# Optimization experiments

Measured on AMD Instinct MI355X. Metric: run time of the kernel, lower is better.

Reference implementation:

```python
import jax, jax.numpy as jnp
import numpy as np

B, C, H, W = 1, 320, 64, 64
HEADS, DH = 8, 40            # inner_dim = 320
CTX_LEN, CTX_DIM = 77, 768
FF_MULT = 4
GN_GROUPS, GN_EPS = 32, 1e-6
LN_EPS = 1e-5
SCALE = DH ** -0.5
WSTD = 0.02


def setup_inputs() -> dict:
    key = jax.random.key(0)
    ks = iter(jax.random.split(key, 32))
    rn = lambda *s: jax.random.normal(next(ks), s, dtype=jnp.float32)
    D = HEADS * DH  # 320
    inp = {
        'hidden_states': rn(B, C, H, W),
        'encoder_hidden_states': rn(B, CTX_LEN, CTX_DIM),
        'gn_g': jnp.ones((C,), jnp.float32), 'gn_b': jnp.zeros((C,), jnp.float32),
        'pi_w': rn(C, D) * WSTD, 'pi_b': jnp.zeros((D,), jnp.float32),
        'n1_g': jnp.ones((D,), jnp.float32), 'n1_b': jnp.zeros((D,), jnp.float32),
        'a1_q': rn(D, D) * WSTD, 'a1_k': rn(D, D) * WSTD, 'a1_v': rn(D, D) * WSTD,
        'a1_o': rn(D, D) * WSTD, 'a1_ob': jnp.zeros((D,), jnp.float32),
        'n2_g': jnp.ones((D,), jnp.float32), 'n2_b': jnp.zeros((D,), jnp.float32),
        'a2_q': rn(D, D) * WSTD, 'a2_k': rn(CTX_DIM, D) * WSTD, 'a2_v': rn(CTX_DIM, D) * WSTD,
        'a2_o': rn(D, D) * WSTD, 'a2_ob': jnp.zeros((D,), jnp.float32),
        'n3_g': jnp.ones((D,), jnp.float32), 'n3_b': jnp.zeros((D,), jnp.float32),
        'ff_w1': rn(D, 2 * FF_MULT * D) * WSTD, 'ff_b1': jnp.zeros((2 * FF_MULT * D,), jnp.float32),
        'ff_w2': rn(FF_MULT * D, D) * WSTD, 'ff_b2': jnp.zeros((D,), jnp.float32),
        'po_w': rn(D, C) * WSTD, 'po_b': jnp.zeros((C,), jnp.float32),
    }
    return inp


def _group_norm(x, g, b):
    # x: [B,C,H,W]
    Bx, Cx, Hx, Wx = x.shape
    xr = x.reshape(Bx, GN_GROUPS, Cx // GN_GROUPS, Hx, Wx)
    mu = xr.mean(axis=(2, 3, 4), keepdims=True)
    var = xr.var(axis=(2, 3, 4), keepdims=True)
    xr = (xr - mu) * jax.lax.rsqrt(var + GN_EPS)
    x = xr.reshape(Bx, Cx, Hx, Wx)
    return x * g[None, :, None, None] + b[None, :, None, None]


def _layer_norm(x, g, b):
    mu = x.mean(-1, keepdims=True)
    var = x.var(-1, keepdims=True)
    return (x - mu) * jax.lax.rsqrt(var + LN_EPS) * g + b


def _attention(x, ctx, wq, wk, wv, wo, bo):
    # x: [B,S,D]; ctx: [B,T,Dc]. Same math as the torch sliced loop
    # (the 2-row slicing changes only execution order, not values).
    Bx, S, D = x.shape
    q = (x @ wq).reshape(Bx, S, HEADS, DH)
    k = (ctx @ wk).reshape(Bx, -1, HEADS, DH)
    v = (ctx @ wv).reshape(Bx, -1, HEADS, DH)
    s = jnp.einsum('bihd,bjhd->bhij', q, k) * SCALE
    p = jax.nn.softmax(s, axis=-1)
    o = jnp.einsum('bhij,bjhd->bihd', p, v).reshape(Bx, S, D)
    return o @ wo + bo


def reference(hidden_states, encoder_hidden_states, gn_g, gn_b, pi_w, pi_b,
              n1_g, n1_b, a1_q, a1_k, a1_v, a1_o, a1_ob,
              n2_g, n2_b, a2_q, a2_k, a2_v, a2_o, a2_ob,
              n3_g, n3_b, ff_w1, ff_b1, ff_w2, ff_b2, po_w, po_b):
    residual = hidden_states
    h = _group_norm(hidden_states, gn_g, gn_b)
    # proj_in: 1x1 conv == per-pixel linear; to [B, HW, D]
    h = jnp.einsum('bchw,cd->bhwd', h, pi_w) + pi_b
    Bx, Hx, Wx, D = h.shape
    h = h.reshape(Bx, Hx * Wx, D)

    # transformer block
    nh = _layer_norm(h, n1_g, n1_b)
    h = h + _attention(nh, nh, a1_q, a1_k, a1_v, a1_o, a1_ob)
    nh = _layer_norm(h, n2_g, n2_b)
    h = h + _attention(nh, encoder_hidden_states, a2_q, a2_k, a2_v, a2_o, a2_ob)
    nh = _layer_norm(h, n3_g, n3_b)
    hg = nh @ ff_w1 + ff_b1
    a, gate = jnp.split(hg, 2, axis=-1)  # GEGLU
    h = h + (a * jax.nn.gelu(gate, approximate=False)) @ ff_w2 + ff_b2

    # proj_out 1x1 conv then residual
    h = h.reshape(Bx, Hx, Wx, D)
    out = jnp.einsum('bhwd,dc->bchw', h, po_w) + po_b[None, :, None, None]
    return out + residual
```

## Files before the change

kernel.cpp:

```cpp
#include <hip/hip_runtime.h>

typedef __bf16 bf16x8 __attribute__((ext_vector_type(8)));
typedef __bf16 bf16x4 __attribute__((ext_vector_type(4)));
typedef __bf16 bf16x2 __attribute__((ext_vector_type(2)));
typedef float f32x4 __attribute__((ext_vector_type(4)));
typedef float f32x16 __attribute__((ext_vector_type(16)));

#define MFMA16(a, b, c) __builtin_amdgcn_mfma_f32_16x16x32_bf16(a, b, c, 0, 0, 0)
#define MFMA32(a, b, c) __builtin_amdgcn_mfma_f32_32x32x16_bf16(a, b, c, 0, 0, 0)

static constexpr float QSCALE = 0.15811388300841897f * 1.4426950408889634f;

__device__ __forceinline__ float fexp2(float x) { return __builtin_amdgcn_exp2f(x); }

__device__ __forceinline__ void gload16(const __bf16* g, __bf16* l) {
  __builtin_amdgcn_global_load_lds((const __attribute__((address_space(1))) void*)g,
                                   (__attribute__((address_space(3))) void*)l, 16, 0, 0);
}

__device__ __forceinline__ bf16x8 zero8() {
  bf16x8 z;
#pragma unroll
  for (int j = 0; j < 8; ++j) z[j] = (__bf16)0.0f;
  return z;
}

__device__ __forceinline__ bf16x8 ones8() {
  bf16x8 z;
#pragma unroll
  for (int j = 0; j < 8; ++j) z[j] = (__bf16)1.0f;
  return z;
}

__device__ __forceinline__ float gelu_exact(float x) {
  return 0.5f * x * (1.0f + erff(x * 0.70710678118654752f));
}

struct WDesc { const float* src; __bf16* dst; int K; int N; int ldn; int noff; };
struct WTable { WDesc w[12]; };

__global__ __launch_bounds__(256) void prep_kernel(WTable tab,
                                                   const float* __restrict__ X,
                                                   float* __restrict__ part) {
  __shared__ float rs[4], rs2[4];
  int id = blockIdx.x;
  if (id < 4800) {
    WDesc d = tab.w[id / 400];
    int total = (d.K >> 3) * d.N;
    int idx = (id % 400) * 256 + threadIdx.x;
    if (idx >= total) return;
    int kb = idx / d.N, n = idx - kb * d.N;
    bf16x8 o;
#pragma unroll
    for (int j = 0; j < 8; ++j) o[j] = (__bf16)d.src[(size_t)(kb * 8 + j) * d.N + n];
    *(bf16x8*)&d.dst[((size_t)kb * d.ldn + d.noff + n) * 8] = o;
  } else {
    int gb = id - 4800;
    int g = gb >> 3, cid = gb & 7;
    const float* base = X + (size_t)g * 40960 + (size_t)cid * 5120;
    int t = threadIdx.x;
    float s = 0.f, s2 = 0.f;
#pragma unroll
    for (int i = t; i < 1280; i += 256) {
      float4 v = ((const float4*)base)[i];
      s += v.x + v.y + v.z + v.w;
      s2 += v.x * v.x + v.y * v.y + v.z * v.z + v.w * v.w;
    }
#pragma unroll
    for (int off = 1; off < 64; off <<= 1) { s += __shfl_xor(s, off); s2 += __shfl_xor(s2, off); }
    int wid = t >> 6, lane = t & 63;
    if (lane == 0) { rs[wid] = s; rs2[wid] = s2; }
    __syncthreads();
    if (t == 0) {
      part[gb * 2] = rs[0] + rs[1] + rs[2] + rs[3];
      part[gb * 2 + 1] = rs2[0] + rs2[1] + rs2[2] + rs2[3];
    }
  }
}

__global__ __launch_bounds__(256) void gn_apply(const float* __restrict__ X,
                                                const float* __restrict__ part,
                                                const float* __restrict__ gg,
                                                const float* __restrict__ gb,
                                                __bf16* __restrict__ Y) {
  int i0 = (blockIdx.x * 256 + threadIdx.x) * 8;
  int c = i0 >> 12, px = i0 & 4095;
  int g = c / 10;
  float s = 0.f, s2 = 0.f;
#pragma unroll
  for (int j = 0; j < 8; ++j) { s += part[(g * 8 + j) * 2]; s2 += part[(g * 8 + j) * 2 + 1]; }
  float mu = s * (1.f / 40960.f);
  float rstd = rsqrtf(s2 * (1.f / 40960.f) - mu * mu + 1e-6f);
  float ga = gg[c] * rstd, bb = gb[c] - mu * ga;
  float4 a = *(const float4*)&X[i0];
  float4 b = *(const float4*)&X[i0 + 4];
  Y[(size_t)(px + 0) * 320 + c] = (__bf16)(a.x * ga + bb);
  Y[(size_t)(px + 1) * 320 + c] = (__bf16)(a.y * ga + bb);
  Y[(size_t)(px + 2) * 320 + c] = (__bf16)(a.z * ga + bb);
  Y[(size_t)(px + 3) * 320 + c] = (__bf16)(a.w * ga + bb);
  Y[(size_t)(px + 4) * 320 + c] = (__bf16)(b.x * ga + bb);
  Y[(size_t)(px + 5) * 320 + c] = (__bf16)(b.y * ga + bb);
  Y[(size_t)(px + 6) * 320 + c] = (__bf16)(b.z * ga + bb);
  Y[(size_t)(px + 7) * 320 + c] = (__bf16)(b.w * ga + bb);
}

__global__ __launch_bounds__(256) void ln_kernel(const float* __restrict__ X,
                                                 const float* __restrict__ g,
                                                 const float* __restrict__ b,
                                                 __bf16* __restrict__ Y) {
  int row = blockIdx.x * 4 + (threadIdx.x >> 6);
  int lane = threadIdx.x & 63;
  const float* x = X + (size_t)row * 320;
  float v[5];
  float s = 0.f;
#pragma unroll
  for (int i = 0; i < 5; ++i) { v[i] = x[lane + 64 * i]; s += v[i]; }
#pragma unroll
  for (int off = 1; off < 64; off <<= 1) s += __shfl_xor(s, off);
  float mu = s * (1.f / 320.f);
  float s2 = 0.f;
#pragma unroll
  for (int i = 0; i < 5; ++i) { float d = v[i] - mu; s2 += d * d; }
#pragma unroll
  for (int off = 1; off < 64; off <<= 1) s2 += __shfl_xor(s2, off);
  float rstd = rsqrtf(s2 * (1.f / 320.f) + 1e-5f);
#pragma unroll
  for (int i = 0; i < 5; ++i) {
    int c = lane + 64 * i;
    Y[(size_t)row * 320 + c] = (__bf16)((v[i] - mu) * rstd * g[c] + b[c]);
  }
}

template <int OM, bool HB, bool HR, bool QS, bool AH>
__global__ __launch_bounds__(256) void gemm32(const __bf16* __restrict__ A,
                                              const __bf16* __restrict__ Bt,
                                              const float* __restrict__ bias,
                                              const float* __restrict__ res,
                                              void* __restrict__ Cout,
                                              void* __restrict__ Cout2,
                                              int M, int N, int K) {
  __shared__ __align__(16) __bf16 sA[2][2048];
  __shared__ __align__(16) __bf16 sB[2][4096];
  int t = threadIdx.x, lane = t & 63, wid = t >> 6;
  int wr = wid >> 1, wc = wid & 1, kb4 = lane >> 4, l15 = lane & 15;
  int id = blockIdx.x;
  int id2 = (id & 7) * 80 + (id >> 3);
  int bx = id2 / 5, by = id2 - bx * 5;
  int m0 = bx * 32, n0 = by * 64;
  const size_t N8 = (size_t)N * 8;
  f32x4 acc[2] = {};
  int r0 = t >> 3, c0 = (t & 7) ^ (r0 & 7);

  auto stage = [&](int buf, int k0) {
    const __bf16* ga0;
    if (AH) {
      int kk = k0 + c0 * 8;
      int hh = kk / 40, dh = kk - hh * 40;
      ga0 = &A[((size_t)hh * 4096 + m0 + r0) * 40 + dh];
    } else {
      ga0 = &A[(size_t)(m0 + r0) * K + k0 + c0 * 8];
    }
    gload16(ga0, &sA[buf][wid * 512]);
    gload16(&Bt[((size_t)(k0 >> 3) + wid) * N8 + (size_t)(n0 + lane) * 8], &sB[buf][wid * 512]);
    gload16(&Bt[((size_t)(k0 >> 3) + wid + 4) * N8 + (size_t)(n0 + lane) * 8], &sB[buf][2048 + wid * 512]);
  };
  stage(0, 0);
  __syncthreads();
  int cur = 0;
  for (int k0 = 0; k0 < K; k0 += 64) {
    if (k0 + 64 < K) stage(cur ^ 1, k0 + 64);
#pragma unroll
    for (int kk = 0; kk < 2; ++kk) {
      int c8 = kb4 + kk * 4;
      int row = wr * 16 + l15;
      bf16x8 af = *(const bf16x8*)&sA[cur][row * 64 + ((c8 * 8) ^ ((row & 7) << 3))];
      bf16x8 bfr[2];
#pragma unroll
      for (int fn = 0; fn < 2; ++fn)
        bfr[fn] = *(const bf16x8*)&sB[cur][(c8 * 64 + wc * 32 + fn * 16 + l15) * 8];
#pragma unroll
      for (int fn = 0; fn < 2; ++fn) acc[fn] = MFMA16(af, bfr[fn], acc[fn]);
    }
    __syncthreads();
    cur ^= 1;
  }
#pragma unroll
  for (int fn = 0; fn < 2; ++fn)
#pragma unroll
    for (int r = 0; r < 4; ++r) {
      int row = m0 + wr * 16 + kb4 * 4 + r;
      int col = n0 + wc * 32 + fn * 16 + l15;
      float v = acc[fn][r];
      if (HB) v += bias[col];
      if (OM == 3) {
        if (HR) v += res[(size_t)col * M + row];
        ((float*)Cout)[(size_t)col * M + row] = v;
      } else if (OM == 4) {
        int hh = col / 40, dh = col - hh * 40;
        __bf16* qp = (__bf16*)Cout + ((size_t)hh * 4096 + row) * 48 + dh;
        *qp = (__bf16)(QS ? v * QSCALE : v);
        if (dh >= 32) qp[8] = (__bf16)0.f;
      } else {
        if (HR) v += res[(size_t)row * N + col];
        if (OM == 0) {
          ((float*)Cout)[(size_t)row * N + col] = v;
        } else if (OM == 1) {
          ((__bf16*)Cout)[(size_t)row * N + col] = (__bf16)(QS ? v * QSCALE : v);
        } else {
          ((float*)Cout)[(size_t)row * N + col] = v;
          ((__bf16*)Cout2)[(size_t)row * N + col] = (__bf16)v;
        }
      }
    }
}

__device__ __forceinline__ void scatterK(__bf16* Kf, int NT, int hh, int row, int dh, float v) {
  int tile = row >> 6, kg = (row >> 5) & 1, k31 = row & 31;
  int s = dh >> 4, hi = (dh >> 3) & 1, j = dh & 7;
  size_t base = (((size_t)hh * NT + tile) * 2 + kg) * 3;
  Kf[(base + s) * 512 + (hi * 32 + k31) * 8 + j] = (__bf16)v;
  if (dh >= 32)
    Kf[(base + 2) * 512 + (32 + k31) * 8 + (dh & 7)] = (__bf16)0.f;
}
__device__ __forceinline__ void scatterV(__bf16* Vfl, __bf16* Vfh, int NT, int hh,
                                         int row, int dh, float v) {
  int tile = row >> 6, kg = (row >> 5) & 1, klo = row & 31;
  int m = (klo >> 4) & 1, hik = (klo >> 2) & 1;
  int jj = (klo & 3) | (((klo >> 3) & 1) << 2);
  size_t base = (((size_t)hh * NT + tile) * 2 + kg) * 2 + m;
  if (dh < 32) Vfl[base * 512 + (hik * 32 + dh) * 8 + jj] = (__bf16)v;
  else Vfh[base * 128 + (hik * 8 + (dh - 32)) * 8 + jj] = (__bf16)v;
}

__global__ __launch_bounds__(256) void qkv_gemm(const __bf16* __restrict__ A,
                                                const __bf16* __restrict__ Bt,
                                                __bf16* __restrict__ Qh,
                                                __bf16* __restrict__ Kf,
                                                __bf16* __restrict__ Vfl,
                                                __bf16* __restrict__ Vfh,
                                                const float* __restrict__ ctx,
                                                const __bf16* __restrict__ wKV2,
                                                __bf16* __restrict__ Kf2,
                                                __bf16* __restrict__ Vfl2,
                                                __bf16* __restrict__ Vfh2) {
  __shared__ __align__(16) char smem[32768];
  __bf16* sA = (__bf16*)smem;
  __bf16* sB = (__bf16*)(smem + 16384);
  int t = threadIdx.x, lane = t & 63, wid = t >> 6;
  int wr = wid >> 1, wc = wid & 1, kb4 = lane >> 4, l15 = lane & 15;

  if (blockIdx.x < 960) {
    int id = blockIdx.x;
    int id2 = (id & 7) * 120 + (id >> 3);
    int bx = id2 / 15, by = id2 - bx * 15;
    int m0 = bx * 64, n0 = by * 64;
    f32x4 acc[2][2] = {};
    int r0 = t >> 3, c0 = (t & 7) ^ (r0 & 7);

    auto stage = [&](int buf, int k0) {
      gload16(&A[(size_t)(m0 + r0) * 320 + k0 + c0 * 8], &sA[buf * 4096 + wid * 512]);
      gload16(&A[(size_t)(m0 + 32 + r0) * 320 + k0 + c0 * 8], &sA[buf * 4096 + 2048 + wid * 512]);
      gload16(&Bt[((size_t)(k0 >> 3) + wid) * (960 * 8) + (size_t)(n0 + lane) * 8], &sB[buf * 4096 + wid * 512]);
      gload16(&Bt[((size_t)(k0 >> 3) + wid + 4) * (960 * 8) + (size_t)(n0 + lane) * 8], &sB[buf * 4096 + 2048 + wid * 512]);
    };
    stage(0, 0);
    __syncthreads();
    int cur = 0;
    for (int k0 = 0; k0 < 320; k0 += 64) {
      if (k0 + 64 < 320) stage(cur ^ 1, k0 + 64);
#pragma unroll
      for (int kk = 0; kk < 2; ++kk) {
        int c8 = kb4 + kk * 4;
        bf16x8 af[2], bfr[2];
#pragma unroll
        for (int fm = 0; fm < 2; ++fm) {
          int row = wr * 32 + fm * 16 + l15;
          af[fm] = *(const bf16x8*)&sA[cur * 4096 + row * 64 + ((c8 * 8) ^ ((row & 7) << 3))];
        }
#pragma unroll
        for (int fn = 0; fn < 2; ++fn)
          bfr[fn] = *(const bf16x8*)&sB[cur * 4096 + (c8 * 64 + wc * 32 + fn * 16 + l15) * 8];
#pragma unroll
        for (int fm = 0; fm < 2; ++fm)
#pragma unroll
          for (int fn = 0; fn < 2; ++fn) acc[fm][fn] = MFMA16(af[fm], bfr[fn], acc[fm][fn]);
      }
      __syncthreads();
      cur ^= 1;
    }
#pragma unroll
    for (int fm = 0; fm < 2; ++fm)
#pragma unroll
      for (int fn = 0; fn < 2; ++fn)
#pragma unroll
        for (int r = 0; r < 4; ++r) {
          int row = m0 + wr * 32 + fm * 16 + kb4 * 4 + r;
          int col = n0 + wc * 32 + fn * 16 + l15;
          float v = acc[fm][fn][r];
          if (col < 320) {
            int hh = col / 40, dh = col - hh * 40;
            __bf16* qp = &Qh[((size_t)hh * 4096 + row) * 48 + dh];
            *qp = (__bf16)(v * QSCALE);
            if (dh >= 32) qp[8] = (__bf16)0.f;
          } else if (col < 640) {
            int d = col - 320;
            int hh = d / 40, dh = d - hh * 40;
            scatterK(Kf, 64, hh, row, dh, v);
          } else {
            int d = col - 640;
            int hh = d / 40, dh = d - hh * 40;
            scatterV(Vfl, Vfh, 64, hh, row, dh, v);
          }
        }
  } else {
    int id2 = blockIdx.x - 960;
    int bx = id2 & 1, by = id2 >> 1;
    int m0 = bx * 64, n0 = by * 64;
    int am = t & 63, ac8 = t >> 6;
    int bn = t & 63, bkb = t >> 6;
    f32x4 acc[2][2] = {};
    bf16x8 rA, rB;
    auto loadA = [&](int k0) -> bf16x8 {
      if (m0 + am < 77) {
        const float* src = &ctx[(size_t)(m0 + am) * 768 + k0 + ac8 * 8];
        float4 x = *(const float4*)src;
        float4 y = *(const float4*)(src + 4);
        bf16x8 o;
        o[0] = (__bf16)x.x; o[1] = (__bf16)x.y; o[2] = (__bf16)x.z; o[3] = (__bf16)x.w;
        o[4] = (__bf16)y.x; o[5] = (__bf16)y.y; o[6] = (__bf16)y.z; o[7] = (__bf16)y.w;
        return o;
      }
      return zero8();
    };
    auto loadB = [&](int k0) {
      return *(const bf16x8*)&wKV2[((size_t)(k0 >> 3) + bkb) * (640 * 8) + (size_t)(n0 + bn) * 8];
    };
    rA = loadA(0); rB = loadB(0);
    *(bf16x8*)&sA[ac8 * 512 + am * 8] = rA;
    *(bf16x8*)&sB[bkb * 512 + bn * 8] = rB;
    __syncthreads();
    int cur = 0;
    for (int k0 = 0; k0 < 768; k0 += 32, cur ^= 1) {
      bool more = (k0 + 32) < 768;
      if (more) { rA = loadA(k0 + 32); rB = loadB(k0 + 32); }
      bf16x8 af[2], bfr[2];
#pragma unroll
      for (int fm = 0; fm < 2; ++fm)
        af[fm] = *(const bf16x8*)&sA[cur * 2048 + kb4 * 512 + (wr * 32 + fm * 16 + l15) * 8];
#pragma unroll
      for (int fn = 0; fn < 2; ++fn)
        bfr[fn] = *(const bf16x8*)&sB[cur * 2048 + kb4 * 512 + (wc * 32 + fn * 16 + l15) * 8];
#pragma unroll
      for (int fm = 0; fm < 2; ++fm)
#pragma unroll
        for (int fn = 0; fn < 2; ++fn) acc[fm][fn] = MFMA16(af[fm], bfr[fn], acc[fm][fn]);
      if (more) {
        *(bf16x8*)&sA[(cur ^ 1) * 2048 + ac8 * 512 + am * 8] = rA;
        *(bf16x8*)&sB[(cur ^ 1) * 2048 + bkb * 512 + bn * 8] = rB;
      }
      __syncthreads();
    }
#pragma unroll
    for (int fm = 0; fm < 2; ++fm)
#pragma unroll
      for (int fn = 0; fn < 2; ++fn)
#pragma unroll
        for (int r = 0; r < 4; ++r) {
          int row = m0 + wr * 32 + fm * 16 + kb4 * 4 + r;
          int col = n0 + wc * 32 + fn * 16 + l15;
          float v = acc[fm][fn][r];
          if (col < 320) {
            int hh = col / 40, dh = col - hh * 40;
            scatterK(Kf2, 2, hh, row, dh, v);
          } else {
            int d = col - 320;
            int hh = d / 40, dh = d - hh * 40;
            scatterV(Vfl2, Vfh2, 2, hh, row, dh, v);
          }
        }
  }
}

__global__ __launch_bounds__(256) void geglu64(const __bf16* __restrict__ A,
                                               const __bf16* __restrict__ Bt,
                                               const float* __restrict__ bias,
                                               __bf16* __restrict__ Out) {
  __shared__ __align__(16) __bf16 sA[2][4096];
  __shared__ __align__(16) __bf16 sB[2][4096];
  __shared__ __align__(16) __bf16 sBg[2][4096];
  int t = threadIdx.x, lane = t & 63, wid = t >> 6;
  int wr = wid >> 1, wc = wid & 1, kb4 = lane >> 4, l15 = lane & 15;
  int id = blockIdx.x;
  int id2 = (id & 7) * 160 + (id >> 3);
  int bx = id2 / 20, by = id2 - bx * 20;
  int m0 = bx * 64, n0 = by * 64;
  f32x4 acc_a[2][2] = {}, acc_g[2][2] = {};
  int r0 = t >> 3, c0 = (t & 7) ^ (r0 & 7);

  auto stage = [&](int buf, int k0) {
    gload16(&A[(size_t)(m0 + r0) * 320 + k0 + c0 * 8], &sA[buf][wid * 512]);
    gload16(&A[(size_t)(m0 + 32 + r0) * 320 + k0 + c0 * 8], &sA[buf][2048 + wid * 512]);
    gload16(&Bt[((size_t)(k0 >> 3) + wid) * (2560 * 8) + (size_t)(n0 + lane) * 8], &sB[buf][wid * 512]);
    gload16(&Bt[((size_t)(k0 >> 3) + wid + 4) * (2560 * 8) + (size_t)(n0 + lane) * 8], &sB[buf][2048 + wid * 512]);
    gload16(&Bt[((size_t)(k0 >> 3) + wid) * (2560 * 8) + (size_t)(1280 + n0 + lane) * 8], &sBg[buf][wid * 512]);
    gload16(&Bt[((size_t)(k0 >> 3) + wid + 4) * (2560 * 8) + (size_t)(1280 + n0 + lane) * 8], &sBg[buf][2048 + wid * 512]);
  };
  stage(0, 0);
  __syncthreads();
  int cur = 0;
  for (int k0 = 0; k0 < 320; k0 += 64) {
    if (k0 + 64 < 320) stage(cur ^ 1, k0 + 64);
#pragma unroll
    for (int kk = 0; kk < 2; ++kk) {
      int c8 = kb4 + kk * 4;
      bf16x8 af[2], bfa[2], bfg[2];
#pragma unroll
      for (int fm = 0; fm < 2; ++fm) {
        int row = wr * 32 + fm * 16 + l15;
        af[fm] = *(const bf16x8*)&sA[cur][row * 64 + ((c8 * 8) ^ ((row & 7) << 3))];
      }
#pragma unroll
      for (int fn = 0; fn < 2; ++fn) {
        bfa[fn] = *(const bf16x8*)&sB[cur][(c8 * 64 + wc * 32 + fn * 16 + l15) * 8];
        bfg[fn] = *(const bf16x8*)&sBg[cur][(c8 * 64 + wc * 32 + fn * 16 + l15) * 8];
      }
#pragma unroll
      for (int fm = 0; fm < 2; ++fm)
#pragma unroll
        for (int fn = 0; fn < 2; ++fn) {
          acc_a[fm][fn] = MFMA16(af[fm], bfa[fn], acc_a[fm][fn]);
          acc_g[fm][fn] = MFMA16(af[fm], bfg[fn], acc_g[fm][fn]);
        }
    }
    __syncthreads();
    cur ^= 1;
  }
#pragma unroll
  for (int fm = 0; fm < 2; ++fm)
#pragma unroll
    for (int fn = 0; fn < 2; ++fn)
#pragma unroll
      for (int r = 0; r < 4; ++r) {
        int row = m0 + wr * 32 + fm * 16 + kb4 * 4 + r;
        int col = n0 + wc * 32 + fn * 16 + l15;
        float a = acc_a[fm][fn][r] + bias[col];
        float g = acc_g[fm][fn][r] + bias[1280 + col];
        Out[(size_t)row * 1280 + col] = (__bf16)(a * gelu_exact(g));
      }
}

__global__ __launch_bounds__(512) void attn_kernel(const __bf16* __restrict__ Qh,
                                                   const __bf16* __restrict__ Kf,
                                                   const __bf16* __restrict__ Vfl,
                                                   const __bf16* __restrict__ Vfh,
                                                   __bf16* __restrict__ Oh,
                                                   int kv_len, int NT) {
  __shared__ float sO[12288];
  int t = threadIdx.x, lane = t & 63, wid = t >> 6;
  int zz = wid >> 1, kg = wid & 1;
  int l31 = lane & 31, hi = lane >> 5;
  int id2 = ((blockIdx.x & 7) << 6) | (blockIdx.x >> 3);
  int h = id2 >> 6, q0 = (id2 & 63) * 64;

  bf16x8 qf0[3], qf1[3];
  {
    const __bf16* qr0 = Qh + ((size_t)h * 4096 + q0 + l31) * 48;
    const __bf16* qr1 = Qh + ((size_t)h * 4096 + q0 + 32 + l31) * 48;
#pragma unroll
    for (int s = 0; s < 3; ++s) {
      qf0[s] = *(const bf16x8*)(qr0 + s * 16 + hi * 8);
      qf1[s] = *(const bf16x8*)(qr1 + s * 16 + hi * 8);
    }
  }
  bf16x8 vfill = (l31 == 8) ? ones8() : zero8();
  f32x16 oL0 = {}, oH0 = {}, oL1 = {}, oH1 = {};

  int half = (NT >= 4) ? (NT >> 2) : 1;
  int t0 = zz * half; if (t0 > NT) t0 = NT;
  int t1 = t0 + half; if (t1 > NT) t1 = NT;
  for (int tile = t0; tile < t1; ++tile) {
    size_t kb = ((size_t)h * NT + tile) * 2 + kg;
    const __bf16* kp = Kf + kb * 1536 + lane * 8;
    bf16x8 kf0 = *(const bf16x8*)(kp);
    bf16x8 kf1 = *(const bf16x8*)(kp + 512);
    bf16x8 kf2 = *(const bf16x8*)(kp + 1024);
    const __bf16* vp = Vfl + kb * 1024 + lane * 8;
    bf16x8 vl0 = *(const bf16x8*)(vp);
    bf16x8 vl1 = *(const bf16x8*)(vp + 512);
    bf16x8 vh0 = vfill, vh1 = vfill;
    if (l31 < 8) {
      const __bf16* vph = Vfh + kb * 256 + (hi * 8 + l31) * 8;
      vh0 = *(const bf16x8*)(vph);
      vh1 = *(const bf16x8*)(vph + 128);
    }
    f32x16 s0 = {}, s1 = {};
    __builtin_amdgcn_s_setprio(1);
    s0 = MFMA32(kf0, qf0[0], s0);
    s1 = MFMA32(kf0, qf1[0], s1);
    s0 = MFMA32(kf1, qf0[1], s0);
    s1 = MFMA32(kf1, qf1[1], s1);
    s0 = MFMA32(kf2, qf0[2], s0);
    s1 = MFMA32(kf2, qf1[2], s1);
    __builtin_amdgcn_s_setprio(0);
    int k0 = tile << 6;
    if (k0 + 64 > kv_len) {
#pragma unroll
      for (int r = 0; r < 16; ++r) {
        int klo = (r & 3) + 8 * (r >> 2) + 4 * hi;
        if (k0 + kg * 32 + klo >= kv_len) { s0[r] = -1e30f; s1[r] = -1e30f; }
      }
    }
    bf16x8 p00, p01, p10, p11;
#pragma unroll
    for (int j = 0; j < 8; ++j) {
      p00[j] = (__bf16)fexp2(s0[j]);
      p01[j] = (__bf16)fexp2(s0[8 + j]);
      p10[j] = (__bf16)fexp2(s1[j]);
      p11[j] = (__bf16)fexp2(s1[8 + j]);
    }
    __builtin_amdgcn_s_setprio(1);
    oL0 = MFMA32(vl0, p00, oL0);
    oL1 = MFMA32(vl0, p10, oL1);
    oH0 = MFMA32(vh0, p00, oH0);
    oH1 = MFMA32(vh0, p10, oH1);
    oL0 = MFMA32(vl1, p01, oL0);
    oL1 = MFMA32(vl1, p11, oL1);
    oH0 = MFMA32(vh1, p01, oH0);
    oH1 = MFMA32(vh1, p11, oH1);
    __builtin_amdgcn_s_setprio(0);
  }
  int srcid = zz * 2 + kg;
  auto dumpTo = [&](int slot, const f32x16& ol, const f32x16& oh, int qg) {
    float* dst = sO + (((size_t)slot * 2 + qg) * 64 + lane) * 24;
#pragma unroll
    for (int r = 0; r < 16; ++r) dst[r] = ol[r];
#pragma unroll
    for (int r = 0; r < 4; ++r) dst[16 + r] = oh[r];
    dst[20] = oh[4];
  };
  auto addFrom = [&](int slot, f32x16& ol, f32x16& oh, int qg) {
    const float* sp = sO + (((size_t)slot * 2 + qg) * 64 + lane) * 24;
#pragma unroll
    for (int r = 0; r < 16; ++r) ol[r] += sp[r];
#pragma unroll
    for (int r = 0; r < 4; ++r) oh[r] += sp[16 + r];
    oh[4] += sp[20];
  };
  if (srcid >= 4) { dumpTo(srcid - 4, oL0, oH0, 0); dumpTo(srcid - 4, oL1, oH1, 1); }
  __syncthreads();
  if (srcid < 4) { addFrom(srcid, oL0, oH0, 0); addFrom(srcid, oL1, oH1, 1); }
  __syncthreads();
  if (srcid >= 1 && srcid < 4) { dumpTo(srcid - 1, oL0, oH0, 0); dumpTo(srcid - 1, oL1, oH1, 1); }
  __syncthreads();
  if (srcid == 0) {
#pragma unroll
    for (int src = 0; src < 3; ++src) { addFrom(src, oL0, oH0, 0); addFrom(src, oL1, oH1, 1); }
#pragma unroll
    for (int qg = 0; qg < 2; ++qg) {
      const f32x16& ol = qg ? oL1 : oL0;
      const f32x16& oh = qg ? oH1 : oH0;
      float ls = __shfl(oh[4], l31);
      float inv = 1.0f / ls;
      __bf16* orow = Oh + ((size_t)h * 4096 + q0 + qg * 32 + l31) * 40;
#pragma unroll
      for (int r = 0; r < 16; r += 2) {
        int d = (r & 3) + 8 * (r >> 2) + 4 * hi;
        bf16x2 o2;
        o2[0] = (__bf16)(ol[r] * inv);
        o2[1] = (__bf16)(ol[r + 1] * inv);
        *(bf16x2*)(orow + d) = o2;
      }
#pragma unroll
      for (int r = 0; r < 4; r += 2) {
        int d = 32 + r + 4 * hi;
        bf16x2 o2;
        o2[0] = (__bf16)(oh[r] * inv);
        o2[1] = (__bf16)(oh[r + 1] * inv);
        *(bf16x2*)(orow + d) = o2;
      }
    }
  }
}

extern "C" void kernel_launch(void* const* d_in, const int* in_sizes, int n_in,
                              void* d_out, int out_size, void* d_ws, size_t ws_size,
                              hipStream_t stream) {
  const float* hs    = (const float*)d_in[0];
  const float* ctx   = (const float*)d_in[1];
  const float* gn_g  = (const float*)d_in[2];
  const float* gn_b  = (const float*)d_in[3];
  const float* pi_w  = (const float*)d_in[4];
  const float* pi_b  = (const float*)d_in[5];
  const float* n1_g  = (const float*)d_in[6];
  const float* n1_b  = (const float*)d_in[7];
  const float* a1_q  = (const float*)d_in[8];
  const float* a1_k  = (const float*)d_in[9];
  const float* a1_v  = (const float*)d_in[10];
  const float* a1_o  = (const float*)d_in[11];
  const float* a1_ob = (const float*)d_in[12];
  const float* n2_g  = (const float*)d_in[13];
  const float* n2_b  = (const float*)d_in[14];
  const float* a2_q  = (const float*)d_in[15];
  const float* a2_k  = (const float*)d_in[16];
  const float* a2_v  = (const float*)d_in[17];
  const float* a2_o  = (const float*)d_in[18];
  const float* a2_ob = (const float*)d_in[19];
  const float* n3_g  = (const float*)d_in[20];
  const float* n3_b  = (const float*)d_in[21];
  const float* ff_w1 = (const float*)d_in[22];
  const float* ff_b1 = (const float*)d_in[23];
  const float* ff_w2 = (const float*)d_in[24];
  const float* ff_b2 = (const float*)d_in[25];
  const float* po_w  = (const float*)d_in[26];
  const float* po_b  = (const float*)d_in[27];

  char* p = (char*)d_ws;
  auto alloc = [&](size_t bytes) {
    char* r = p;
    p += (bytes + 255) & ~(size_t)255;
    return r;
  };
  __bf16* wPI  = (__bf16*)alloc((size_t)320 * 320 * 2);
  __bf16* wQKV = (__bf16*)alloc((size_t)320 * 960 * 2);
  __bf16* wO1  = (__bf16*)alloc((size_t)320 * 320 * 2);
  __bf16* wQ2  = (__bf16*)alloc((size_t)320 * 320 * 2);
  __bf16* wKV2 = (__bf16*)alloc((size_t)768 * 640 * 2);
  __bf16* wO2  = (__bf16*)alloc((size_t)320 * 320 * 2);
  __bf16* wFF1 = (__bf16*)alloc((size_t)320 * 2560 * 2);
  __bf16* wFF2 = (__bf16*)alloc((size_t)1280 * 320 * 2);
  __bf16* wPO  = (__bf16*)alloc((size_t)320 * 320 * 2);

  float*  gpart= (float*)alloc((size_t)256 * 2 * 4);
  __bf16* xg   = (__bf16*)alloc((size_t)4096 * 320 * 2);
  float*  h    = (float*)alloc((size_t)4096 * 320 * 4);
  __bf16* hb   = (__bf16*)alloc((size_t)4096 * 320 * 2);
  __bf16* nx   = (__bf16*)alloc((size_t)4096 * 320 * 2);
  __bf16* qh   = (__bf16*)alloc((size_t)8 * 4096 * 48 * 2);
  __bf16* kf   = (__bf16*)alloc((size_t)8 * 64 * 2 * 3 * 512 * 2);
  __bf16* vfl  = (__bf16*)alloc((size_t)8 * 64 * 2 * 2 * 512 * 2);
  __bf16* vfh  = (__bf16*)alloc((size_t)8 * 64 * 2 * 2 * 128 * 2);
  __bf16* kf2  = (__bf16*)alloc((size_t)8 * 2 * 2 * 3 * 512 * 2);
  __bf16* vfl2 = (__bf16*)alloc((size_t)8 * 2 * 2 * 2 * 512 * 2);
  __bf16* vfh2 = (__bf16*)alloc((size_t)8 * 2 * 2 * 2 * 128 * 2);
  __bf16* oh   = (__bf16*)alloc((size_t)4096 * 320 * 2);
  __bf16* g    = (__bf16*)alloc((size_t)4096 * 1280 * 2);
  float*  outp = (float*)d_out;

  WTable tab;
  tab.w[0]  = WDesc{pi_w,  wPI,  320, 320, 320, 0};
  tab.w[1]  = WDesc{a1_q,  wQKV, 320, 320, 960, 0};
  tab.w[2]  = WDesc{a1_k,  wQKV, 320, 320, 960, 320};
  tab.w[3]  = WDesc{a1_v,  wQKV, 320, 320, 960, 640};
  tab.w[4]  = WDesc{a1_o,  wO1,  320, 320, 320, 0};
  tab.w[5]  = WDesc{a2_q,  wQ2,  320, 320, 320, 0};
  tab.w[6]  = WDesc{a2_k,  wKV2, 768, 320, 640, 0};
  tab.w[7]  = WDesc{a2_v,  wKV2, 768, 320, 640, 320};
  tab.w[8]  = WDesc{a2_o,  wO2,  320, 320, 320, 0};
  tab.w[9]  = WDesc{ff_w1, wFF1, 320, 2560, 2560, 0};
  tab.w[10] = WDesc{ff_w2, wFF2, 1280, 320, 320, 0};
  tab.w[11] = WDesc{po_w,  wPO,  320, 320, 320, 0};
  prep_kernel<<<dim3(5056), 256, 0, stream>>>(tab, hs, gpart);
  gn_apply<<<dim3(640), 256, 0, stream>>>(hs, gpart, gn_g, gn_b, xg);
  gemm32<0, true, false, false, false><<<dim3(640), 256, 0, stream>>>(xg, wPI, pi_b, nullptr, h, nullptr, 4096, 320, 320);
  ln_kernel<<<dim3(1024), 256, 0, stream>>>(h, n1_g, n1_b, nx);
  qkv_gemm<<<dim3(980), 256, 0, stream>>>(nx, wQKV, qh, kf, vfl, vfh,
                                          ctx, wKV2, kf2, vfl2, vfh2);
  attn_kernel<<<dim3(512), 512, 0, stream>>>(qh, kf, vfl, vfh, oh, 4096, 64);
  gemm32<0, true, true, false, true><<<dim3(640), 256, 0, stream>>>(oh, wO1, a1_ob, h, h, nullptr, 4096, 320, 320);
  ln_kernel<<<dim3(1024), 256, 0, stream>>>(h, n2_g, n2_b, nx);
  gemm32<4, false, false, true, false><<<dim3(640), 256, 0, stream>>>(nx, wQ2, nullptr, nullptr, qh, nullptr, 4096, 320, 320);
  attn_kernel<<<dim3(512), 512, 0, stream>>>(qh, kf2, vfl2, vfh2, oh, 77, 2);
  gemm32<0, true, true, false, true><<<dim3(640), 256, 0, stream>>>(oh, wO2, a2_ob, h, h, nullptr, 4096, 320, 320);
  ln_kernel<<<dim3(1024), 256, 0, stream>>>(h, n3_g, n3_b, nx);
  geglu64<<<dim3(1280), 256, 0, stream>>>(nx, wFF1, ff_b1, g);
  gemm32<2, true, true, false, false><<<dim3(640), 256, 0, stream>>>(g, wFF2, ff_b2, h, h, hb, 4096, 320, 1280);
  gemm32<3, true, true, false, false><<<dim3(640), 256, 0, stream>>>(hb, wPO, po_b, hs, outp, nullptr, 4096, 320, 320);
}
```

Baseline: 155.9 us.

## Fuse LayerNorm into neighbouring GEMMs via epilogue row stats and prologue normalization

Removes the three standalone LayerNorm kernels. Producing GEMMs now accumulate per-row sum and sum of squares into a zeroed stats buffer with atomics in their epilogue. Consuming GEMMs (qkv, q2, geglu) read the fp32 residual rows, normalize them on the fly and store bf16 into LDS instead of loading a precomputed bf16 buffer. This saves three launches and the round trip through the normalized buffer. In exchange it adds atomics, switches variance to the one-pass E[x²]-mu² form, and repeats the normalization work across N-tiles with synchronous fp32 loads in the staging path.

```diff
diff --git a/kernel.cpp b/kernel.cpp
--- a/kernel.cpp
+++ b/kernel.cpp
@@ -36,12 +36,39 @@
   return 0.5f * x * (1.0f + erff(x * 0.70710678118654752f));
 }
 
+__device__ __forceinline__ bf16x8 ln8(const float* hrow, int c, float mu, float rstd,
+                                      const float* g, const float* b) {
+  float4 x = *(const float4*)(hrow + c);
+  float4 y = *(const float4*)(hrow + c + 4);
+  float4 g0 = *(const float4*)(g + c);
+  float4 g1 = *(const float4*)(g + c + 4);
+  float4 b0 = *(const float4*)(b + c);
+  float4 b1 = *(const float4*)(b + c + 4);
+  bf16x8 o;
+  o[0] = (__bf16)((x.x - mu) * rstd * g0.x + b0.x);
+  o[1] = (__bf16)((x.y - mu) * rstd * g0.y + b0.y);
+  o[2] = (__bf16)((x.z - mu) * rstd * g0.z + b0.z);
+  o[3] = (__bf16)((x.w - mu) * rstd * g0.w + b0.w);
+  o[4] = (__bf16)((y.x - mu) * rstd * g1.x + b1.x);
+  o[5] = (__bf16)((y.y - mu) * rstd * g1.y + b1.y);
+  o[6] = (__bf16)((y.z - mu) * rstd * g1.z + b1.z);
+  o[7] = (__bf16)((y.w - mu) * rstd * g1.w + b1.w);
+  return o;
+}
+
+__device__ __forceinline__ void rowstat(const float* rs, int row, float& mu, float& rstd) {
+  float2 st = *(const float2*)&rs[row * 2];
+  mu = st.x * (1.f / 320.f);
+  rstd = rsqrtf(st.y * (1.f / 320.f) - mu * mu + 1e-5f);
+}
+
 struct WDesc { const float* src; __bf16* dst; int K; int N; int ldn; int noff; };
 struct WTable { WDesc w[12]; };
 
 __global__ __launch_bounds__(256) void prep_kernel(WTable tab,
                                                    const float* __restrict__ X,
-                                                   float* __restrict__ part) {
+                                                   float* __restrict__ part,
+                                                   float* __restrict__ rsall) {
   __shared__ float rs[4], rs2[4];
   int id = blockIdx.x;
   if (id < 4800) {
@@ -54,7 +81,7 @@
 #pragma unroll
     for (int j = 0; j < 8; ++j) o[j] = (__bf16)d.src[(size_t)(kb * 8 + j) * d.N + n];
     *(bf16x8*)&d.dst[((size_t)kb * d.ldn + d.noff + n) * 8] = o;
-  } else {
+  } else if (id < 5056) {
     int gb = id - 4800;
     int g = gb >> 3, cid = gb & 7;
     const float* base = X + (size_t)g * 40960 + (size_t)cid * 5120;
@@ -75,6 +102,12 @@
       part[gb * 2] = rs[0] + rs[1] + rs[2] + rs[3];
       part[gb * 2 + 1] = rs2[0] + rs2[1] + rs2[2] + rs2[3];
     }
+  } else {
+    int zb = id - 5056;
+    float4 z = {0.f, 0.f, 0.f, 0.f};
+    float* dst = rsall + ((size_t)zb * 256 + threadIdx.x) * 8;
+    *(float4*)dst = z;
+    *(float4*)(dst + 4) = z;
   }
 }
 
@@ -104,41 +137,19 @@
   Y[(size_t)(px + 7) * 320 + c] = (__bf16)(b.w * ga + bb);
 }
 
-__global__ __launch_bounds__(256) void ln_kernel(const float* __restrict__ X,
-                                                 const float* __restrict__ g,
-                                                 const float* __restrict__ b,
-                                                 __bf16* __restrict__ Y) {
-  int row = blockIdx.x * 4 + (threadIdx.x >> 6);
-  int lane = threadIdx.x & 63;
-  const float* x = X + (size_t)row * 320;
-  float v[5];
-  float s = 0.f;
-#pragma unroll
-  for (int i = 0; i < 5; ++i) { v[i] = x[lane + 64 * i]; s += v[i]; }
-#pragma unroll
-  for (int off = 1; off < 64; off <<= 1) s += __shfl_xor(s, off);
-  float mu = s * (1.f / 320.f);
-  float s2 = 0.f;
-#pragma unroll
-  for (int i = 0; i < 5; ++i) { float d = v[i] - mu; s2 += d * d; }
-#pragma unroll
-  for (int off = 1; off < 64; off <<= 1) s2 += __shfl_xor(s2, off);
-  float rstd = rsqrtf(s2 * (1.f / 320.f) + 1e-5f);
-#pragma unroll
-  for (int i = 0; i < 5; ++i) {
-    int c = lane + 64 * i;
-    Y[(size_t)row * 320 + c] = (__bf16)((v[i] - mu) * rstd * g[c] + b[c]);
-  }
-}
-
-template <int OM, bool HB, bool HR, bool QS, bool AH>
+template <int OM, bool HB, bool HR, bool QS, bool AH, bool ST, bool LNA>
 __global__ __launch_bounds__(256) void gemm32(const __bf16* __restrict__ A,
                                               const __bf16* __restrict__ Bt,
                                               const float* __restrict__ bias,
                                               const float* __restrict__ res,
                                               void* __restrict__ Cout,
                                               void* __restrict__ Cout2,
-                                              int M, int N, int K) {
+                                              int M, int N, int K,
+                                              float* __restrict__ rso,
+                                              const float* __restrict__ Hsrc,
+                                              const float* __restrict__ rsi,
+                                              const float* __restrict__ lng,
+                                              const float* __restrict__ lnb) {
   __shared__ __align__(16) __bf16 sA[2][2048];
   __shared__ __align__(16) __bf16 sB[2][4096];
   int t = threadIdx.x, lane = t & 63, wid = t >> 6;
@@ -151,16 +162,24 @@
   f32x4 acc[2] = {};
   int r0 = t >> 3, c0 = (t & 7) ^ (r0 & 7);
 
+  float muA = 0.f, rstdA = 0.f;
+  if (LNA) rowstat(rsi, m0 + r0, muA, rstdA);
+
   auto stage = [&](int buf, int k0) {
-    const __bf16* ga0;
-    if (AH) {
-      int kk = k0 + c0 * 8;
-      int hh = kk / 40, dh = kk - hh * 40;
-      ga0 = &A[((size_t)hh * 4096 + m0 + r0) * 40 + dh];
+    if (LNA) {
+      const float* hrow = Hsrc + (size_t)(m0 + r0) * 320;
+      *(bf16x8*)&sA[buf][(size_t)t * 8] = ln8(hrow, k0 + c0 * 8, muA, rstdA, lng, lnb);
     } else {
-      ga0 = &A[(size_t)(m0 + r0) * K + k0 + c0 * 8];
-    }
-    gload16(ga0, &sA[buf][wid * 512]);
+      const __bf16* ga0;
+      if (AH) {
+        int kk = k0 + c0 * 8;
+        int hh = kk / 40, dh = kk - hh * 40;
+        ga0 = &A[((size_t)hh * 4096 + m0 + r0) * 40 + dh];
+      } else {
+        ga0 = &A[(size_t)(m0 + r0) * K + k0 + c0 * 8];
+      }
+      gload16(ga0, &sA[buf][wid * 512]);
+    }
     gload16(&Bt[((size_t)(k0 >> 3) + wid) * N8 + (size_t)(n0 + lane) * 8], &sB[buf][wid * 512]);
     gload16(&Bt[((size_t)(k0 >> 3) + wid + 4) * N8 + (size_t)(n0 + lane) * 8], &sB[buf][2048 + wid * 512]);
   };
@@ -185,10 +204,11 @@
     cur ^= 1;
   }
 #pragma unroll
-  for (int fn = 0; fn < 2; ++fn)
-#pragma unroll
-    for (int r = 0; r < 4; ++r) {
-      int row = m0 + wr * 16 + kb4 * 4 + r;
+  for (int r = 0; r < 4; ++r) {
+    float sv = 0.f, sv2 = 0.f;
+    int row = m0 + wr * 16 + kb4 * 4 + r;
+#pragma unroll
+    for (int fn = 0; fn < 2; ++fn) {
       int col = n0 + wc * 32 + fn * 16 + l15;
       float v = acc[fn][r];
       if (HB) v += bias[col];
@@ -211,7 +231,20 @@
           ((__bf16*)Cout2)[(size_t)row * N + col] = (__bf16)v;
         }
       }
-    }
+      if (ST) { sv += v; sv2 += v * v; }
+    }
+    if (ST) {
+#pragma unroll
+      for (int off = 1; off < 16; off <<= 1) {
+        sv += __shfl_xor(sv, off);
+        sv2 += __shfl_xor(sv2, off);
+      }
+      if (l15 == 0) {
+        atomicAdd(&rso[row * 2], sv);
+        atomicAdd(&rso[row * 2 + 1], sv2);
+      }
+    }
+  }
 }
 
 __device__ __forceinline__ void scatterK(__bf16* Kf, int NT, int hh, int row, int dh, float v) {
@@ -232,7 +265,10 @@
   else Vfh[base * 128 + (hik * 8 + (dh - 32)) * 8 + jj] = (__bf16)v;
 }
 
-__global__ __launch_bounds__(256) void qkv_gemm(const __bf16* __restrict__ A,
+__global__ __launch_bounds__(256) void qkv_gemm(const float* __restrict__ Hsrc,
+                                                const float* __restrict__ rsi,
+                                                const float* __restrict__ lng,
+                                                const float* __restrict__ lnb,
                                                 const __bf16* __restrict__ Bt,
                                                 __bf16* __restrict__ Qh,
                                                 __bf16* __restrict__ Kf,
@@ -256,10 +292,16 @@
     int m0 = bx * 64, n0 = by * 64;
     f32x4 acc[2][2] = {};
     int r0 = t >> 3, c0 = (t & 7) ^ (r0 & 7);
+    float muA, rstdA, muB, rstdB;
+    rowstat(rsi, m0 + r0, muA, rstdA);
+    rowstat(rsi, m0 + 32 + r0, muB, rstdB);
+    const float* hrowA = Hsrc + (size_t)(m0 + r0) * 320;
+    const float* hrowB = Hsrc + (size_t)(m0 + 32 + r0) * 320;
 
     auto stage = [&](int buf, int k0) {
-      gload16(&A[(size_t)(m0 + r0) * 320 + k0 + c0 * 8], &sA[buf * 4096 + wid * 512]);
-      gload16(&A[(size_t)(m0 + 32 + r0) * 320 + k0 + c0 * 8], &sA[buf * 4096 + 2048 + wid * 512]);
+      int c = k0 + c0 * 8;
+      *(bf16x8*)&sA[buf * 4096 + (size_t)t * 8] = ln8(hrowA, c, muA, rstdA, lng, lnb);
+      *(bf16x8*)&sA[buf * 4096 + 2048 + (size_t)t * 8] = ln8(hrowB, c, muB, rstdB, lng, lnb);
       gload16(&Bt[((size_t)(k0 >> 3) + wid) * (960 * 8) + (size_t)(n0 + lane) * 8], &sB[buf * 4096 + wid * 512]);
       gload16(&Bt[((size_t)(k0 >> 3) + wid + 4) * (960 * 8) + (size_t)(n0 + lane) * 8], &sB[buf * 4096 + 2048 + wid * 512]);
     };
@@ -381,7 +423,10 @@
   }
 }
 
-__global__ __launch_bounds__(256) void geglu64(const __bf16* __restrict__ A,
+__global__ __launch_bounds__(256) void geglu64(const float* __restrict__ Hsrc,
+                                               const float* __restrict__ rsi,
+                                               const float* __restrict__ lng,
+                                               const float* __restrict__ lnb,
                                                const __bf16* __restrict__ Bt,
                                                const float* __restrict__ bias,
                                                __bf16* __restrict__ Out) {
@@ -396,10 +441,16 @@
   int m0 = bx * 64, n0 = by * 64;
   f32x4 acc_a[2][2] = {}, acc_g[2][2] = {};
   int r0 = t >> 3, c0 = (t & 7) ^ (r0 & 7);
+  float muA, rstdA, muB, rstdB;
+  rowstat(rsi, m0 + r0, muA, rstdA);
+  rowstat(rsi, m0 + 32 + r0, muB, rstdB);
+  const float* hrowA = Hsrc + (size_t)(m0 + r0) * 320;
+  const float* hrowB = Hsrc + (size_t)(m0 + 32 + r0) * 320;
 
   auto stage = [&](int buf, int k0) {
-    gload16(&A[(size_t)(m0 + r0) * 320 + k0 + c0 * 8], &sA[buf][wid * 512]);
-    gload16(&A[(size_t)(m0 + 32 + r0) * 320 + k0 + c0 * 8], &sA[buf][2048 + wid * 512]);
+    int c = k0 + c0 * 8;
+    *(bf16x8*)&sA[buf][(size_t)t * 8] = ln8(hrowA, c, muA, rstdA, lng, lnb);
+    *(bf16x8*)&sA[buf][2048 + (size_t)t * 8] = ln8(hrowB, c, muB, rstdB, lng, lnb);
     gload16(&Bt[((size_t)(k0 >> 3) + wid) * (2560 * 8) + (size_t)(n0 + lane) * 8], &sB[buf][wid * 512]);
     gload16(&Bt[((size_t)(k0 >> 3) + wid + 4) * (2560 * 8) + (size_t)(n0 + lane) * 8], &sB[buf][2048 + wid * 512]);
     gload16(&Bt[((size_t)(k0 >> 3) + wid) * (2560 * 8) + (size_t)(1280 + n0 + lane) * 8], &sBg[buf][wid * 512]);
@@ -631,10 +682,13 @@
   __bf16* wPO  = (__bf16*)alloc((size_t)320 * 320 * 2);
 
   float*  gpart= (float*)alloc((size_t)256 * 2 * 4);
+  float*  rsall= (float*)alloc((size_t)24576 * 4);
+  float*  rs1  = rsall;
+  float*  rs2  = rsall + 8192;
+  float*  rs3  = rsall + 16384;
   __bf16* xg   = (__bf16*)alloc((size_t)4096 * 320 * 2);
   float*  h    = (float*)alloc((size_t)4096 * 320 * 4);
   __bf16* hb   = (__bf16*)alloc((size_t)4096 * 320 * 2);
-  __bf16* nx   = (__bf16*)alloc((size_t)4096 * 320 * 2);
   __bf16* qh   = (__bf16*)alloc((size_t)8 * 4096 * 48 * 2);
   __bf16* kf   = (__bf16*)alloc((size_t)8 * 64 * 2 * 3 * 512 * 2);
   __bf16* vfl  = (__bf16*)alloc((size_t)8 * 64 * 2 * 2 * 512 * 2);
@@ -659,20 +713,23 @@
   tab.w[9]  = WDesc{ff_w1, wFF1, 320, 2560, 2560, 0};
   tab.w[10] = WDesc{ff_w2, wFF2, 1280, 320, 320, 0};
   tab.w[11] = WDesc{po_w,  wPO,  320, 320, 320, 0};
-  prep_kernel<<<dim3(5056), 256, 0, stream>>>(tab, hs, gpart);
+  prep_kernel<<<dim3(5068), 256, 0, stream>>>(tab, hs, gpart, rsall);
   gn_apply<<<dim3(640), 256, 0, stream>>>(hs, gpart, gn_g, gn_b, xg);
-  gemm32<0, true, false, false, false><<<dim3(640), 256, 0, stream>>>(xg, wPI, pi_b, nullptr, h, nullptr, 4096, 320, 320);
-  ln_kernel<<<dim3(1024), 256, 0, stream>>>(h, n1_g, n1_b, nx);
-  qkv_gemm<<<dim3(980), 256, 0, stream>>>(nx, wQKV, qh, kf, vfl, vfh,
+  gemm32<0, true, false, false, false, true, false><<<dim3(640), 256, 0, stream>>>(
+      xg, wPI, pi_b, nullptr, h, nullptr, 4096, 320, 320, rs1, nullptr, nullptr, nullptr, nullptr);
+  qkv_gemm<<<dim3(980), 256, 0, stream>>>(h, rs1, n1_g, n1_b, wQKV, qh, kf, vfl, vfh,
                                           ctx, wKV2, kf2, vfl2, vfh2);
   attn_kernel<<<dim3(512), 512, 0, stream>>>(qh, kf, vfl, vfh, oh, 4096, 64);
-  gemm32<0, true, true, false, true><<<dim3(640), 256, 0, stream>>>(oh, wO1, a1_ob, h, h, nullptr, 4096, 320, 320);
-  ln_kernel<<<dim3(1024), 256, 0, stream>>>(h, n2_g, n2_b, nx);
-  gemm32<4, false, false, true, false><<<dim3(640), 256, 0, stream>>>(nx, wQ2, nullptr, nullptr, qh, nullptr, 4096, 320, 320);
+  gemm32<0, true, true, false, true, true, false><<<dim3(640), 256, 0, stream>>>(
+      oh, wO1, a1_ob, h, h, nullptr, 4096, 320, 320, rs2, nullptr, nullptr, nullptr, nullptr);
+  gemm32<4, false, false, true, false, false, true><<<dim3(640), 256, 0, stream>>>(
+      nullptr, wQ2, nullptr, nullptr, qh, nullptr, 4096, 320, 320, nullptr, h, rs2, n2_g, n2_b);
   attn_kernel<<<dim3(512), 512, 0, stream>>>(qh, kf2, vfl2, vfh2, oh, 77, 2);
-  gemm32<0, true, true, false, true><<<dim3(640), 256, 0, stream>>>(oh, wO2, a2_ob, h, h, nullptr, 4096, 320, 320);
-  ln_kernel<<<dim3(1024), 256, 0, stream>>>(h, n3_g, n3_b, nx);
-  geglu64<<<dim3(1280), 256, 0, stream>>>(nx, wFF1, ff_b1, g);
-  gemm32<2, true, true, false, false><<<dim3(640), 256, 0, stream>>>(g, wFF2, ff_b2, h, h, hb, 4096, 320, 1280);
-  gemm32<3, true, true, false, false><<<dim3(640), 256, 0, stream>>>(hb, wPO, po_b, hs, outp, nullptr, 4096, 320, 320);
-}
+  gemm32<0, true, true, false, true, true, false><<<dim3(640), 256, 0, stream>>>(
+      oh, wO2, a2_ob, h, h, nullptr, 4096, 320, 320, rs3, nullptr, nullptr, nullptr, nullptr);
+  geglu64<<<dim3(1280), 256, 0, stream>>>(h, rs3, n3_g, n3_b, wFF1, ff_b1, g);
+  gemm32<2, true, true, false, false, false, false><<<dim3(640), 256, 0, stream>>>(
+      g, wFF2, ff_b2, h, h, hb, 4096, 320, 1280, nullptr, nullptr, nullptr, nullptr, nullptr);
+  gemm32<3, true, true, false, false, false, false><<<dim3(640), 256, 0, stream>>>(
+      hb, wPO, po_b, hs, outp, nullptr, 4096, 320, 320, nullptr, nullptr, nullptr, nullptr, nullptr);
+}
```

After: 157.3 us. About the same (+0.9%).

## Halve attention query tile to 32 rows and double grid size

Applied to the files above, without the earlier changes.

The attention kernel now has each block handle 32 queries instead of 64, and the launch grid doubles from 512 to 1024 blocks. Each wave issues half the MFMAs per KV tile, and the cross-wave reduction becomes a single-stage dump by seven waves followed by accumulation in wave 0, using a tighter 21-float LDS stride. The aim is more blocks to fill the CUs, lower register pressure, and fewer barriers. The cost is that each K/V fragment is loaded twice as often overall, and the final reduction in one wave is serialized.

```diff
diff --git a/kernel.cpp b/kernel.cpp
--- a/kernel.cpp
+++ b/kernel.cpp
@@ -455,29 +455,26 @@
                                                    const __bf16* __restrict__ Vfh,
                                                    __bf16* __restrict__ Oh,
                                                    int kv_len, int NT) {
-  __shared__ float sO[12288];
+  __shared__ float sO[9408];
   int t = threadIdx.x, lane = t & 63, wid = t >> 6;
   int zz = wid >> 1, kg = wid & 1;
   int l31 = lane & 31, hi = lane >> 5;
-  int id2 = ((blockIdx.x & 7) << 6) | (blockIdx.x >> 3);
-  int h = id2 >> 6, q0 = (id2 & 63) * 64;
-
-  bf16x8 qf0[3], qf1[3];
+  int id2 = ((blockIdx.x & 7) << 7) | (blockIdx.x >> 3);
+  int h = id2 >> 7, q0 = (id2 & 127) * 32;
+  int q = q0 + l31;
+
+  bf16x8 qf[3];
   {
-    const __bf16* qr0 = Qh + ((size_t)h * 4096 + q0 + l31) * 48;
-    const __bf16* qr1 = Qh + ((size_t)h * 4096 + q0 + 32 + l31) * 48;
-#pragma unroll
-    for (int s = 0; s < 3; ++s) {
-      qf0[s] = *(const bf16x8*)(qr0 + s * 16 + hi * 8);
-      qf1[s] = *(const bf16x8*)(qr1 + s * 16 + hi * 8);
-    }
+    const __bf16* qrow = Qh + ((size_t)h * 4096 + q) * 48;
+#pragma unroll
+    for (int s = 0; s < 3; ++s) qf[s] = *(const bf16x8*)(qrow + s * 16 + hi * 8);
   }
   bf16x8 vfill = (l31 == 8) ? ones8() : zero8();
-  f32x16 oL0 = {}, oH0 = {}, oL1 = {}, oH1 = {};
-
-  int half = (NT >= 4) ? (NT >> 2) : 1;
-  int t0 = zz * half; if (t0 > NT) t0 = NT;
-  int t1 = t0 + half; if (t1 > NT) t1 = NT;
+  f32x16 o_lo = {}, o_hi = {};
+
+  int quarter = (NT >= 4) ? (NT >> 2) : 1;
+  int t0 = zz * quarter; if (t0 > NT) t0 = NT;
+  int t1 = t0 + quarter; if (t1 > NT) t1 = NT;
   for (int tile = t0; tile < t1; ++tile) {
     size_t kb = ((size_t)h * NT + tile) * 2 + kg;
     const __bf16* kp = Kf + kb * 1536 + lane * 8;
@@ -493,91 +490,71 @@
       vh0 = *(const bf16x8*)(vph);
       vh1 = *(const bf16x8*)(vph + 128);
     }
-    f32x16 s0 = {}, s1 = {};
+    f32x16 s = {};
     __builtin_amdgcn_s_setprio(1);
-    s0 = MFMA32(kf0, qf0[0], s0);
-    s1 = MFMA32(kf0, qf1[0], s1);
-    s0 = MFMA32(kf1, qf0[1], s0);
-    s1 = MFMA32(kf1, qf1[1], s1);
-    s0 = MFMA32(kf2, qf0[2], s0);
-    s1 = MFMA32(kf2, qf1[2], s1);
+    s = MFMA32(kf0, qf[0], s);
+    s = MFMA32(kf1, qf[1], s);
+    s = MFMA32(kf2, qf[2], s);
     __builtin_amdgcn_s_setprio(0);
     int k0 = tile << 6;
     if (k0 + 64 > kv_len) {
 #pragma unroll
       for (int r = 0; r < 16; ++r) {
         int klo = (r & 3) + 8 * (r >> 2) + 4 * hi;
-        if (k0 + kg * 32 + klo >= kv_len) { s0[r] = -1e30f; s1[r] = -1e30f; }
-      }
-    }
-    bf16x8 p00, p01, p10, p11;
+        if (k0 + kg * 32 + klo >= kv_len) s[r] = -1e30f;
+      }
+    }
+    bf16x8 p0, p1;
 #pragma unroll
     for (int j = 0; j < 8; ++j) {
-      p00[j] = (__bf16)fexp2(s0[j]);
-      p01[j] = (__bf16)fexp2(s0[8 + j]);
-      p10[j] = (__bf16)fexp2(s1[j]);
-      p11[j] = (__bf16)fexp2(s1[8 + j]);
+      p0[j] = (__bf16)fexp2(s[j]);
+      p1[j] = (__bf16)fexp2(s[8 + j]);
     }
     __builtin_amdgcn_s_setprio(1);
-    oL0 = MFMA32(vl0, p00, oL0);
-    oL1 = MFMA32(vl0, p10, oL1);
-    oH0 = MFMA32(vh0, p00, oH0);
-    oH1 = MFMA32(vh0, p10, oH1);
-    oL0 = MFMA32(vl1, p01, oL0);
-    oL1 = MFMA32(vl1, p11, oL1);
-    oH0 = MFMA32(vh1, p01, oH0);
-    oH1 = MFMA32(vh1, p11, oH1);
+    o_lo = MFMA32(vl0, p0, o_lo);
+    o_hi = MFMA32(vh0, p0, o_hi);
+    o_lo = MFMA32(vl1, p1, o_lo);
+    o_hi = MFMA32(vh1, p1, o_hi);
     __builtin_amdgcn_s_setprio(0);
   }
   int srcid = zz * 2 + kg;
-  auto dumpTo = [&](int slot, const f32x16& ol, const f32x16& oh, int qg) {
-    float* dst = sO + (((size_t)slot * 2 + qg) * 64 + lane) * 24;
-#pragma unroll
-    for (int r = 0; r < 16; ++r) dst[r] = ol[r];
-#pragma unroll
-    for (int r = 0; r < 4; ++r) dst[16 + r] = oh[r];
-    dst[20] = oh[4];
-  };
-  auto addFrom = [&](int slot, f32x16& ol, f32x16& oh, int qg) {
-    const float* sp = sO + (((size_t)slot * 2 + qg) * 64 + lane) * 24;
-#pragma unroll
-    for (int r = 0; r < 16; ++r) ol[r] += sp[r];
-#pragma unroll
-    for (int r = 0; r < 4; ++r) oh[r] += sp[16 + r];
-    oh[4] += sp[20];
-  };
-  if (srcid >= 4) { dumpTo(srcid - 4, oL0, oH0, 0); dumpTo(srcid - 4, oL1, oH1, 1); }
-  __syncthreads();
-  if (srcid < 4) { addFrom(srcid, oL0, oH0, 0); addFrom(srcid, oL1, oH1, 1); }
-  __syncthreads();
-  if (srcid >= 1 && srcid < 4) { dumpTo(srcid - 1, oL0, oH0, 0); dumpTo(srcid - 1, oL1, oH1, 1); }
+  if (srcid != 0) {
+    float* dst = sO + (((size_t)(srcid - 1)) * 64 + lane) * 21;
+#pragma unroll
+    for (int r = 0; r < 16; ++r) dst[r] = o_lo[r];
+#pragma unroll
+    for (int r = 0; r < 4; ++r) dst[16 + r] = o_hi[r];
+    dst[20] = o_hi[4];
+  }
   __syncthreads();
   if (srcid == 0) {
 #pragma unroll
-    for (int src = 0; src < 3; ++src) { addFrom(src, oL0, oH0, 0); addFrom(src, oL1, oH1, 1); }
-#pragma unroll
-    for (int qg = 0; qg < 2; ++qg) {
-      const f32x16& ol = qg ? oL1 : oL0;
-      const f32x16& oh = qg ? oH1 : oH0;
-      float ls = __shfl(oh[4], l31);
-      float inv = 1.0f / ls;
-      __bf16* orow = Oh + ((size_t)h * 4096 + q0 + qg * 32 + l31) * 40;
-#pragma unroll
-      for (int r = 0; r < 16; r += 2) {
-        int d = (r & 3) + 8 * (r >> 2) + 4 * hi;
-        bf16x2 o2;
-        o2[0] = (__bf16)(ol[r] * inv);
-        o2[1] = (__bf16)(ol[r + 1] * inv);
-        *(bf16x2*)(orow + d) = o2;
-      }
-#pragma unroll
-      for (int r = 0; r < 4; r += 2) {
-        int d = 32 + r + 4 * hi;
-        bf16x2 o2;
-        o2[0] = (__bf16)(oh[r] * inv);
-        o2[1] = (__bf16)(oh[r + 1] * inv);
-        *(bf16x2*)(orow + d) = o2;
-      }
+    for (int src = 0; src < 7; ++src) {
+      const float* sp = sO + (((size_t)src) * 64 + lane) * 21;
+#pragma unroll
+      for (int r = 0; r < 16; ++r) o_lo[r] += sp[r];
+#pragma unroll
+      for (int r = 0; r < 4; ++r) o_hi[r] += sp[16 + r];
+      o_hi[4] += sp[20];
+    }
+    float ls = __shfl(o_hi[4], l31);
+    float inv = 1.0f / ls;
+    __bf16* orow = Oh + ((size_t)h * 4096 + q) * 40;
+#pragma unroll
+    for (int r = 0; r < 16; r += 2) {
+      int d = (r & 3) + 8 * (r >> 2) + 4 * hi;
+      bf16x2 o2;
+      o2[0] = (__bf16)(o_lo[r] * inv);
+      o2[1] = (__bf16)(o_lo[r + 1] * inv);
+      *(bf16x2*)(orow + d) = o2;
+    }
+#pragma unroll
+    for (int r = 0; r < 4; r += 2) {
+      int d = 32 + r + 4 * hi;
+      bf16x2 o2;
+      o2[0] = (__bf16)(o_hi[r] * inv);
+      o2[1] = (__bf16)(o_hi[r + 1] * inv);
+      *(bf16x2*)(orow + d) = o2;
     }
   }
 }
@@ -665,11 +642,11 @@
   ln_kernel<<<dim3(1024), 256, 0, stream>>>(h, n1_g, n1_b, nx);
   qkv_gemm<<<dim3(980), 256, 0, stream>>>(nx, wQKV, qh, kf, vfl, vfh,
                                           ctx, wKV2, kf2, vfl2, vfh2);
-  attn_kernel<<<dim3(512), 512, 0, stream>>>(qh, kf, vfl, vfh, oh, 4096, 64);
+  attn_kernel<<<dim3(1024), 512, 0, stream>>>(qh, kf, vfl, vfh, oh, 4096, 64);
   gemm32<0, true, true, false, true><<<dim3(640), 256, 0, stream>>>(oh, wO1, a1_ob, h, h, nullptr, 4096, 320, 320);
   ln_kernel<<<dim3(1024), 256, 0, stream>>>(h, n2_g, n2_b, nx);
   gemm32<4, false, false, true, false><<<dim3(640), 256, 0, stream>>>(nx, wQ2, nullptr, nullptr, qh, nullptr, 4096, 320, 320);
-  attn_kernel<<<dim3(512), 512, 0, stream>>>(qh, kf2, vfl2, vfh2, oh, 77, 2);
+  attn_kernel<<<dim3(1024), 512, 0, stream>>>(qh, kf2, vfl2, vfh2, oh, 77, 2);
   gemm32<0, true, true, false, true><<<dim3(640), 256, 0, stream>>>(oh, wO2, a2_ob, h, h, nullptr, 4096, 320, 320);
   ln_kernel<<<dim3(1024), 256, 0, stream>>>(h, n3_g, n3_b, nx);
   geglu64<<<dim3(1280), 256, 0, stream>>>(nx, wFF1, ff_b1, g);
```

Result: slower. 159.7 us (+2.5%).
